# Kernel tuning notes

Measured on AMD Instinct MI355X. Metric: run time of the kernel, lower is better.

Reference implementation:

```python
import jax, jax.numpy as jnp
import numpy as np

EPS = 1e-5


def setup_inputs() -> dict:
    key = jax.random.key(0)
    k1, k2, k3, k4 = jax.random.split(key, 4)
    B, C, H, W = 4, 64, 128, 256
    Hg, Wg = 512, 1024
    NC = 19  # num_class; loop also covers ignore label 255 -> NC+1 entries
    x = jax.random.normal(k1, (B, C, H, W), dtype=jnp.float32)
    gt = jax.random.randint(k2, (B, Hg, Wg), 0, 19).astype(jnp.int32)
    eps_mu = jax.random.normal(k3, (NC + 1, B, C), dtype=jnp.float32)
    eps_std = jax.random.normal(k4, (NC + 1, B, C), dtype=jnp.float32)
    return {"x": x, "gt": gt, "eps_mu": eps_mu, "eps_std": eps_std}


def _sqrtvar(t):
    # torch .var(dim=0) is unbiased (ddof=1); repeat over batch is just broadcast
    return jnp.sqrt(jnp.var(t, axis=0, ddof=1, keepdims=True) + EPS)


def reference(x, gt, eps_mu, eps_std):
    B, C, H, W = x.shape
    NC1 = eps_mu.shape[0]  # num_class + 1 (ignore label 255)
    Hg, Wg = gt.shape[1], gt.shape[2]
    # nearest resize of the (binary) mask == compare on nearest-resized labels
    # torch F.interpolate nearest: src = floor(dst * in/out)
    ih = (jnp.arange(H) * Hg) // H
    iw = (jnp.arange(W) * Wg) // W
    gt_r = gt[:, ih[:, None], iw[None, :]]  # [B,H,W]
    class_ids = jnp.concatenate(
        [jnp.arange(NC1 - 1), jnp.array([255])]).astype(gt.dtype)

    def per_class(carry, inp):
        cid, emu, estd = inp
        mask = (gt_r == cid).astype(x.dtype)[:, None]  # [B,1,H,W]
        mx = x * mask
        npx = jnp.sum(mask, axis=(2, 3))               # [B,1]
        npx = jnp.where(npx == 0, jnp.ones_like(npx), npx)
        mean = jnp.sum(mx, axis=(2, 3)) / npx          # [B,C] == mean*wh/npx
        var = jnp.sum((mask * (mx - mean[:, :, None, None])) ** 2,
                      axis=(2, 3)) / npx
        std = jnp.sqrt(var + EPS)                      # [B,C]
        beta = mean + emu * _sqrtvar(mean)
        gamma = std + estd * _sqrtvar(std)
        xn = (mx - mean[:, :, None, None]) / std[:, :, None, None]
        out = mask * (xn * gamma[:, :, None, None] + beta[:, :, None, None])
        return carry + out, None

    class_x, _ = jax.lax.scan(per_class, jnp.zeros_like(x),
                              (class_ids, eps_mu, eps_std))
    return class_x
```

## Files before the change

kernel.cpp:

```cpp
#include <hip/hip_runtime.h>

#define EPS 1e-5f
constexpr int B = 4, C = 64, H = 128, W = 256;
constexpr int Hg = 512, Wg = 1024;
constexpr int NC = 19;
constexpr int HW = H * W;
constexpr int HW4 = HW / 4;

typedef float f32x4 __attribute__((ext_vector_type(4)));

__global__ __launch_bounds__(256) void k_pack(const int* __restrict__ gt,
                                              unsigned int* __restrict__ gt_p,
                                              int* __restrict__ counts_pb) {
  __shared__ int hist[NC];
  int t = threadIdx.x;
  if (t < NC) hist[t] = 0;
  __syncthreads();
  int R = blockIdx.x * 4 + (t >> 6);
  int ws = t & 63;
  int b = R >> 7, h = R & 127;
  const int* row = gt + (size_t)(b * Hg + h * 4) * Wg;
  unsigned int c0 = (unsigned int)row[ws * 16 + 0];
  unsigned int c1 = (unsigned int)row[ws * 16 + 4];
  unsigned int c2 = (unsigned int)row[ws * 16 + 8];
  unsigned int c3 = (unsigned int)row[ws * 16 + 12];
  gt_p[R * 64 + ws] = c0 | (c1 << 8) | (c2 << 16) | (c3 << 24);
  atomicAdd(&hist[c0], 1); atomicAdd(&hist[c1], 1);
  atomicAdd(&hist[c2], 1); atomicAdd(&hist[c3], 1);
  __syncthreads();
  if (t < NC) counts_pb[t * 128 + blockIdx.x] = hist[t];
}

__global__ __launch_bounds__(256) void k_stats(const float* __restrict__ x,
                                               const unsigned int* __restrict__ gt_p,
                                               const int* __restrict__ counts_pb,
                                               float2* __restrict__ par,
                                               int* __restrict__ counts) {
  __shared__ float2 acc[NC * 256];
  int t = threadIdx.x;
  for (int k = t; k < NC * 256; k += 256) acc[k] = make_float2(0.f, 0.f);
  int plane = blockIdx.x >> 2;
  int q = blockIdx.x & 3;
  int b = plane >> 6, c = plane & 63;

  if (c == 0 && q == 0 && t < NC) {
    const int4* cp = (const int4*)&counts_pb[t * 128 + b * 32];
    int s = 0;
#pragma unroll
    for (int j = 0; j < 8; j++) { int4 cv = cp[j]; s += cv.x + cv.y + cv.z + cv.w; }
    counts[b * NC + t] = s;
  }
  __syncthreads();

  const float4* xp = (const float4*)x + (size_t)plane * (HW / 4) + q * 2048;
  const unsigned int* gp = gt_p + (size_t)b * HW4 + q * 2048;
  for (int j = 0; j < 8; j++) {
    int i = j * 256 + t;
    float4 v = xp[i];
    unsigned int g = gp[i];
    int c0 = g & 255, c1 = (g >> 8) & 255, c2 = (g >> 16) & 255, c3 = g >> 24;
    float2 a;
    a = acc[c0 * 256 + t]; a.x += v.x; a.y += v.x * v.x; acc[c0 * 256 + t] = a;
    a = acc[c1 * 256 + t]; a.x += v.y; a.y += v.y * v.y; acc[c1 * 256 + t] = a;
    a = acc[c2 * 256 + t]; a.x += v.z; a.y += v.z * v.z; acc[c2 * 256 + t] = a;
    a = acc[c3 * 256 + t]; a.x += v.w; a.y += v.w * v.w; acc[c3 * 256 + t] = a;
  }
  __syncthreads();

  int w = t >> 6, lane = t & 63;
  for (int k = w; k < NC; k += 4) {
    float2 a0 = acc[k * 256 + lane];
    float2 a1 = acc[k * 256 + 64 + lane];
    float2 a2 = acc[k * 256 + 128 + lane];
    float2 a3 = acc[k * 256 + 192 + lane];
    float s  = a0.x + a1.x + a2.x + a3.x;
    float qq = a0.y + a1.y + a2.y + a3.y;
    for (int m = 32; m >= 1; m >>= 1) {
      s  += __shfl_xor(s, m, 64);
      qq += __shfl_xor(qq, m, 64);
    }
    if (lane == 0) {
      int e = (k * B + b) * C + c;
      par[e * 4 + q] = make_float2(s, qq);
    }
  }
}

__global__ __launch_bounds__(256) void k_apply(const float* __restrict__ x,
                                               const unsigned int* __restrict__ gt_p,
                                               const float2* __restrict__ par,
                                               const int* __restrict__ counts,
                                               const float* __restrict__ eps_mu,
                                               const float* __restrict__ eps_std,
                                               float* __restrict__ out) {
  __shared__ float2 tab[NC];
  int t = threadIdx.x;
  int plane = blockIdx.x >> 2;
  int q = blockIdx.x & 3;
  int b = plane >> 6, c = plane & 63;
  const float4* xp = (const float4*)x + (size_t)plane * (HW / 4) + q * 2048;
  const unsigned int* gp = gt_p + (size_t)b * HW4 + q * 2048;
  f32x4* op = (f32x4*)((float4*)out + (size_t)plane * (HW / 4) + q * 2048);

  float4 v0 = xp[t];
  unsigned int g0 = gp[t];

  if (t < NC) {
    float mean[B], stdv[B];
    float msum = 0.f, ssum = 0.f;
#pragma unroll
    for (int bb = 0; bb < B; bb++) {
      int cnt = counts[bb * NC + t];
      float n = cnt > 0 ? (float)cnt : 1.f;
      const float4* pp = (const float4*)&par[((t * B + bb) * C + c) * 4];
      float4 p0 = pp[0], p1 = pp[1];
      float s  = (p0.x + p0.z) + (p1.x + p1.z);
      float qq = (p0.y + p0.w) + (p1.y + p1.w);
      float m = s / n;
      float var = qq / n - m * m;
      var = var > 0.f ? var : 0.f;
      mean[bb] = m;
      stdv[bb] = sqrtf(var + EPS);
      msum += m; ssum += stdv[bb];
    }
    float mbar = msum * 0.25f, sbar = ssum * 0.25f;
    float vm = 0.f, vs = 0.f;
#pragma unroll
    for (int bb = 0; bb < B; bb++) {
      float dm = mean[bb] - mbar; vm += dm * dm;
      float ds = stdv[bb] - sbar; vs += ds * ds;
    }
    float sqvm = sqrtf(vm * (1.f / 3.f) + EPS);
    float sqvs = sqrtf(vs * (1.f / 3.f) + EPS);
    int e = (t * B + b) * C + c;
    float beta  = mean[b] + eps_mu[e]  * sqvm;
    float gamma = stdv[b] + eps_std[e] * sqvs;
    float sc = gamma / stdv[b];
    tab[t] = make_float2(sc, beta - mean[b] * sc);
  }
  __syncthreads();

  {
    float2 a0 = tab[g0 & 255], a1 = tab[(g0 >> 8) & 255];
    float2 a2 = tab[(g0 >> 16) & 255], a3 = tab[g0 >> 24];
    f32x4 o;
    o.x = fmaf(v0.x, a0.x, a0.y);
    o.y = fmaf(v0.y, a1.x, a1.y);
    o.z = fmaf(v0.z, a2.x, a2.y);
    o.w = fmaf(v0.w, a3.x, a3.y);
    __builtin_nontemporal_store(o, &op[t]);
  }
  for (int j = 1; j < 8; j++) {
    int i = j * 256 + t;
    float4 v = xp[i];
    unsigned int g = gp[i];
    float2 a0 = tab[g & 255], a1 = tab[(g >> 8) & 255];
    float2 a2 = tab[(g >> 16) & 255], a3 = tab[g >> 24];
    f32x4 o;
    o.x = fmaf(v.x, a0.x, a0.y);
    o.y = fmaf(v.y, a1.x, a1.y);
    o.z = fmaf(v.z, a2.x, a2.y);
    o.w = fmaf(v.w, a3.x, a3.y);
    __builtin_nontemporal_store(o, &op[i]);
  }
}

extern "C" void kernel_launch(void* const* d_in, const int* in_sizes, int n_in,
                              void* d_out, int out_size, void* d_ws, size_t ws_size,
                              hipStream_t stream) {
  const float* x       = (const float*)d_in[0];
  const int*   gt      = (const int*)  d_in[1];
  const float* eps_mu  = (const float*)d_in[2];
  const float* eps_std = (const float*)d_in[3];
  float* out = (float*)d_out;

  char* ws = (char*)d_ws;
  unsigned int* gt_p     = (unsigned int*)(ws);
  int*          counts_pb= (int*)   (ws + 131072);
  int*          counts   = (int*)   (ws + 140800);
  float2*       par      = (float2*)(ws + 141104);

  hipLaunchKernelGGL(k_pack,  dim3(B * H / 4), dim3(256), 0, stream, gt, gt_p, counts_pb);
  hipLaunchKernelGGL(k_stats, dim3(B * C * 4), dim3(256), 0, stream,
                     x, gt_p, counts_pb, par, counts);
  hipLaunchKernelGGL(k_apply, dim3(B * C * 4), dim3(256), 0, stream,
                     x, gt_p, par, counts, eps_mu, eps_std, out);
}
```

Before: 102.4 us.

## Fuse label packing and histogram into the stats kernel, dropping the pack launch

```diff
diff --git a/kernel.cpp b/kernel.cpp
--- a/kernel.cpp
+++ b/kernel.cpp
@@ -9,56 +9,42 @@
 
 typedef float f32x4 __attribute__((ext_vector_type(4)));
 
-__global__ __launch_bounds__(256) void k_pack(const int* __restrict__ gt,
-                                              unsigned int* __restrict__ gt_p,
-                                              int* __restrict__ counts_pb) {
+__global__ __launch_bounds__(256) void k_stats(const float* __restrict__ x,
+                                               const int* __restrict__ gt,
+                                               unsigned int* __restrict__ gt_p,
+                                               int* __restrict__ counts_pb,
+                                               float2* __restrict__ par) {
+  __shared__ float2 acc[NC * 256];
   __shared__ int hist[NC];
   int t = threadIdx.x;
+  for (int k = t; k < NC * 256; k += 256) acc[k] = make_float2(0.f, 0.f);
   if (t < NC) hist[t] = 0;
-  __syncthreads();
-  int R = blockIdx.x * 4 + (t >> 6);
-  int ws = t & 63;
-  int b = R >> 7, h = R & 127;
-  const int* row = gt + (size_t)(b * Hg + h * 4) * Wg;
-  unsigned int c0 = (unsigned int)row[ws * 16 + 0];
-  unsigned int c1 = (unsigned int)row[ws * 16 + 4];
-  unsigned int c2 = (unsigned int)row[ws * 16 + 8];
-  unsigned int c3 = (unsigned int)row[ws * 16 + 12];
-  gt_p[R * 64 + ws] = c0 | (c1 << 8) | (c2 << 16) | (c3 << 24);
-  atomicAdd(&hist[c0], 1); atomicAdd(&hist[c1], 1);
-  atomicAdd(&hist[c2], 1); atomicAdd(&hist[c3], 1);
-  __syncthreads();
-  if (t < NC) counts_pb[t * 128 + blockIdx.x] = hist[t];
-}
-
-__global__ __launch_bounds__(256) void k_stats(const float* __restrict__ x,
-                                               const unsigned int* __restrict__ gt_p,
-                                               const int* __restrict__ counts_pb,
-                                               float2* __restrict__ par,
-                                               int* __restrict__ counts) {
-  __shared__ float2 acc[NC * 256];
-  int t = threadIdx.x;
-  for (int k = t; k < NC * 256; k += 256) acc[k] = make_float2(0.f, 0.f);
   int plane = blockIdx.x >> 2;
   int q = blockIdx.x & 3;
   int b = plane >> 6, c = plane & 63;
-
-  if (c == 0 && q == 0 && t < NC) {
-    const int4* cp = (const int4*)&counts_pb[t * 128 + b * 32];
-    int s = 0;
-#pragma unroll
-    for (int j = 0; j < 8; j++) { int4 cv = cp[j]; s += cv.x + cv.y + cv.z + cv.w; }
-    counts[b * NC + t] = s;
-  }
   __syncthreads();
 
   const float4* xp = (const float4*)x + (size_t)plane * (HW / 4) + q * 2048;
-  const unsigned int* gp = gt_p + (size_t)b * HW4 + q * 2048;
+  int ws = t & 63;
+  int h0 = q * 32 + (t >> 6);
+  const int* row = gt + (size_t)(b * Hg + h0 * 4) * Wg + ws * 16;
+  bool writer = (c == 0);
+  unsigned int* gw = gt_p + (size_t)b * HW4 + q * 2048;
+
+#pragma unroll
   for (int j = 0; j < 8; j++) {
     int i = j * 256 + t;
     float4 v = xp[i];
-    unsigned int g = gp[i];
-    int c0 = g & 255, c1 = (g >> 8) & 255, c2 = (g >> 16) & 255, c3 = g >> 24;
+    unsigned int c0 = (unsigned int)row[0];
+    unsigned int c1 = (unsigned int)row[4];
+    unsigned int c2 = (unsigned int)row[8];
+    unsigned int c3 = (unsigned int)row[12];
+    row += 16 * Wg;
+    if (writer) gw[i] = c0 | (c1 << 8) | (c2 << 16) | (c3 << 24);
+    if (c < 8 && j == c) {
+      atomicAdd(&hist[c0], 1); atomicAdd(&hist[c1], 1);
+      atomicAdd(&hist[c2], 1); atomicAdd(&hist[c3], 1);
+    }
     float2 a;
     a = acc[c0 * 256 + t]; a.x += v.x; a.y += v.x * v.x; acc[c0 * 256 + t] = a;
     a = acc[c1 * 256 + t]; a.x += v.y; a.y += v.y * v.y; acc[c1 * 256 + t] = a;
@@ -66,6 +52,8 @@
     a = acc[c3 * 256 + t]; a.x += v.w; a.y += v.w * v.w; acc[c3 * 256 + t] = a;
   }
   __syncthreads();
+
+  if (c < 8 && t < NC) counts_pb[((t * B + b) * 4 + q) * 8 + c] = hist[t];
 
   int w = t >> 6, lane = t & 63;
   for (int k = w; k < NC; k += 4) {
@@ -89,7 +77,7 @@
 __global__ __launch_bounds__(256) void k_apply(const float* __restrict__ x,
                                                const unsigned int* __restrict__ gt_p,
                                                const float2* __restrict__ par,
-                                               const int* __restrict__ counts,
+                                               const int* __restrict__ counts_pb,
                                                const float* __restrict__ eps_mu,
                                                const float* __restrict__ eps_std,
                                                float* __restrict__ out) {
@@ -110,7 +98,10 @@
     float msum = 0.f, ssum = 0.f;
 #pragma unroll
     for (int bb = 0; bb < B; bb++) {
-      int cnt = counts[bb * NC + t];
+      const int4* cp = (const int4*)&counts_pb[(t * B + bb) * 32];
+      int cnt = 0;
+#pragma unroll
+      for (int j = 0; j < 8; j++) { int4 cv = cp[j]; cnt += cv.x + cv.y + cv.z + cv.w; }
       float n = cnt > 0 ? (float)cnt : 1.f;
       const float4* pp = (const float4*)&par[((t * B + bb) * C + c) * 4];
       float4 p0 = pp[0], p1 = pp[1];
@@ -177,12 +168,10 @@
   char* ws = (char*)d_ws;
   unsigned int* gt_p     = (unsigned int*)(ws);
   int*          counts_pb= (int*)   (ws + 131072);
-  int*          counts   = (int*)   (ws + 140800);
-  float2*       par      = (float2*)(ws + 141104);
+  float2*       par      = (float2*)(ws + 140800);
 
-  hipLaunchKernelGGL(k_pack,  dim3(B * H / 4), dim3(256), 0, stream, gt, gt_p, counts_pb);
   hipLaunchKernelGGL(k_stats, dim3(B * C * 4), dim3(256), 0, stream,
-                     x, gt_p, counts_pb, par, counts);
+                     x, gt, gt_p, counts_pb, par);
   hipLaunchKernelGGL(k_apply, dim3(B * C * 4), dim3(256), 0, stream,
-                     x, gt_p, par, counts, eps_mu, eps_std, out);
+                     x, gt_p, par, counts_pb, eps_mu, eps_std, out);
 }
```

Measured after the change: 110.1 us. 7.5% more time.
